# Performance work log

Measured on AMD Instinct MI355X. Metric: run time of the kernel, lower is better.

## Reference

```python
import jax, jax.numpy as jnp
import numpy as np

D_MODEL = 1024
D_STATE = 16
D_CONV = 4
EXPAND = 2
D_INNER = EXPAND * D_MODEL          # 2048
DT_RANK = D_MODEL // 16             # 64
BATCH, SEQ = 4, 2048


def setup_inputs() -> dict:
    key = jax.random.key(0)
    ks = jax.random.split(key, 8)
    s = lambda k, shape, sc=0.02: jax.random.normal(k, shape, jnp.float32) * sc
    x = jax.random.normal(ks[0], (BATCH, SEQ, D_MODEL), jnp.float32)
    tau = jax.random.uniform(ks[1], (BATCH, SEQ), jnp.float32) * 7200.0  # seconds
    # S4D-real init for A
    A_log = jnp.log(jnp.broadcast_to(jnp.arange(1, D_STATE + 1, dtype=jnp.float32), (D_INNER, D_STATE)))
    return dict(
        x=x, tau=tau,
        ln_g=jnp.ones((D_MODEL,), jnp.float32),
        ln_b=jnp.zeros((D_MODEL,), jnp.float32),
        in_proj_w=s(ks[2], (2 * D_INNER, D_MODEL)),
        conv_w=s(ks[3], (D_INNER, 1, D_CONV), 0.1),   # depthwise [O, I/g=1, K]
        conv_b=jnp.zeros((D_INNER,), jnp.float32),
        x_proj_w=s(ks[4], (DT_RANK + 2 * D_STATE, D_INNER)),
        dt_proj_w=s(ks[5], (D_INNER, DT_RANK), 0.1),
        dt_proj_b=jnp.full((D_INNER,), -4.6, jnp.float32),  # softplus ~ 0.01
        A_log=A_log,
        D=jnp.ones((D_INNER,), jnp.float32),
        out_proj_w=s(ks[6], (D_MODEL, D_INNER)),
        log_decay=jnp.full((D_MODEL,), -3.0, jnp.float32),
    )


def _mamba_block(x, tau, ln_g, ln_b, in_proj_w, conv_w, conv_b, x_proj_w,
                 dt_proj_w, dt_proj_b, A_log, D, out_proj_w, log_decay):
    # LayerNorm(d_model)
    mu = jnp.mean(x, axis=-1, keepdims=True)
    var = jnp.var(x, axis=-1, keepdims=True)
    xn = (x - mu) * jax.lax.rsqrt(var + 1e-5) * ln_g + ln_b

    # in_proj -> split into conv branch and gate branch, each [B, L, d_inner]
    xz = jnp.einsum('bld,ed->ble', xn, in_proj_w)
    x_in, z = jnp.split(xz, 2, axis=-1)

    # causal depthwise conv1d over time
    xc = jax.lax.conv_general_dilated(
        x_in.transpose(0, 2, 1), conv_w, (1,), [(D_CONV - 1, 0)],
        dimension_numbers=('NCH', 'OIH', 'NCH'), feature_group_count=D_INNER)
    u = jax.nn.silu(xc.transpose(0, 2, 1) + conv_b)          # [B, L, d_inner]

    # input-dependent SSM params
    x_dbl = jnp.einsum('ble,fe->blf', u, x_proj_w)
    dt, Bm, Cm = jnp.split(x_dbl, [DT_RANK, DT_RANK + D_STATE], axis=-1)
    delta = jax.nn.softplus(jnp.einsum('blr,dr->bld', dt, dt_proj_w) + dt_proj_b)
    A = -jnp.exp(A_log)                                       # [d_inner, d_state]

    # selective scan: h_t = exp(dt*A)*h + dt*u*B_t ; y_t = <h_t, C_t>
    def step(h, inp):
        d_t, B_t, C_t, u_t = inp                              # [B,d],[B,n],[B,n],[B,d]
        h = jnp.exp(d_t[..., None] * A) * h + (d_t * u_t)[..., None] * B_t[:, None, :]
        return h, jnp.einsum('bdn,bn->bd', h, C_t)

    h0 = jnp.zeros((x.shape[0], D_INNER, D_STATE), x.dtype)
    xs = (delta.transpose(1, 0, 2), Bm.transpose(1, 0, 2),
          Cm.transpose(1, 0, 2), u.transpose(1, 0, 2))
    _, ys = jax.lax.scan(step, h0, xs)
    y = ys.transpose(1, 0, 2) + u * D
    y = y * jax.nn.silu(z)
    h_out = jnp.einsum('ble,de->bld', y, out_proj_w)          # mamba output [B,L,d_model]

    # ZOH time-decay gate + residual (dropout = identity in eval)
    tau_h = jnp.maximum(tau / 3600.0, 1e-4)[..., None]
    gate = jnp.exp(-jax.nn.softplus(log_decay) * tau_h)
    return x + h_out * gate


def reference(x, tau, ln_g, ln_b, in_proj_w, conv_w, conv_b, x_proj_w,
              dt_proj_w, dt_proj_b, A_log, D, out_proj_w, log_decay):
    return _mamba_block(x, tau, ln_g, ln_b, in_proj_w, conv_w, conv_b, x_proj_w,
                        dt_proj_w, dt_proj_b, A_log, D, out_proj_w, log_decay)
```

## Files before the change

### kernel.cpp

```cpp
#include <hip/hip_runtime.h>

typedef unsigned short u16;
typedef unsigned int u32;
typedef short s16x8 __attribute__((ext_vector_type(8)));
typedef u16 u16x8 __attribute__((ext_vector_type(8)));
typedef float f32x4 __attribute__((ext_vector_type(4)));

#define TOK 8192
#define DM 1024
#define DI 2048
#define DS 16
#define DR 64
#define NCHUNK 64
#define CH 32
#define XPN 96
#define XP_SPLIT 4
#define CONV_T 16

#define SBAR() do { asm volatile("" ::: "memory"); __builtin_amdgcn_s_barrier(); asm volatile("" ::: "memory"); } while (0)
#define WAITVM(N) do { asm volatile("s_waitcnt vmcnt(" #N ")" ::: "memory"); __builtin_amdgcn_sched_barrier(0); } while (0)
#define WAITLGKM0() do { asm volatile("s_waitcnt lgkmcnt(0)" ::: "memory"); __builtin_amdgcn_sched_barrier(0); } while (0)

__device__ __forceinline__ u16 f2bf(float f) {
    u32 u = __float_as_uint(f);
    u32 r = (u + 0x7fffu + ((u >> 16) & 1u)) >> 16;
    return (u16)r;
}
__device__ __forceinline__ float bf2f(u16 h) {
    return __uint_as_float(((u32)h) << 16);
}
__device__ __forceinline__ float softplus_f(float x) {
    return (x > 15.f) ? x : __logf(1.f + __expf(x));
}
__device__ __forceinline__ void unpack8(const uint4 v, float* o) {
    o[0] = __uint_as_float(v.x << 16); o[1] = __uint_as_float(v.x & 0xffff0000u);
    o[2] = __uint_as_float(v.y << 16); o[3] = __uint_as_float(v.y & 0xffff0000u);
    o[4] = __uint_as_float(v.z << 16); o[5] = __uint_as_float(v.z & 0xffff0000u);
    o[6] = __uint_as_float(v.w << 16); o[7] = __uint_as_float(v.w & 0xffff0000u);
}
__device__ __forceinline__ void async16(u16* lds, const u16* g) {
    __builtin_amdgcn_global_load_lds(
        (const __attribute__((address_space(1))) void*)g,
        (__attribute__((address_space(3))) void*)lds, 16, 0, 0);
}

__global__ __launch_bounds__(256) void cvt_kernel(const float* __restrict__ src,
                                                  u16* __restrict__ dst, int n4) {
    int i = blockIdx.x * 256 + threadIdx.x;
    if (i >= n4) return;
    float4 v = ((const float4*)src)[i];
    ushort4 o;
    o.x = f2bf(v.x); o.y = f2bf(v.y); o.z = f2bf(v.z); o.w = f2bf(v.w);
    ((ushort4*)dst)[i] = o;
}

__global__ __launch_bounds__(256) void prep_kernel(const float* __restrict__ tau,
                                                   const float* __restrict__ log_decay,
                                                   float* __restrict__ th,
                                                   float* __restrict__ sd) {
    int i = blockIdx.x * 256 + threadIdx.x;
    if (i < TOK) th[i] = fmaxf(tau[i] * (1.f / 3600.f), 1e-4f);
    if (i < DM)  sd[i] = softplus_f(log_decay[i]);
}

__global__ __launch_bounds__(256) void ln_kernel(const float* __restrict__ x,
                                                 const float* __restrict__ g,
                                                 const float* __restrict__ bb,
                                                 u16* __restrict__ xn) {
    const int tok = blockIdx.x;
    const float4 v = ((const float4*)(x + (size_t)tok * DM))[threadIdx.x];
    float s = v.x + v.y + v.z + v.w;
    float sq = v.x * v.x + v.y * v.y + v.z * v.z + v.w * v.w;
#pragma unroll
    for (int off = 32; off; off >>= 1) {
        s += __shfl_xor(s, off);
        sq += __shfl_xor(sq, off);
    }
    __shared__ float red[8];
    const int wv = threadIdx.x >> 6;
    if ((threadIdx.x & 63) == 0) { red[wv] = s; red[4 + wv] = sq; }
    __syncthreads();
    s = red[0] + red[1] + red[2] + red[3];
    sq = red[4] + red[5] + red[6] + red[7];
    const float mean = s * (1.f / DM);
    const float var = sq * (1.f / DM) - mean * mean;
    const float rstd = rsqrtf(var + 1e-5f);
    const float4 gv = ((const float4*)g)[threadIdx.x];
    const float4 bv = ((const float4*)bb)[threadIdx.x];
    ushort4 o;
    o.x = f2bf((v.x - mean) * rstd * gv.x + bv.x);
    o.y = f2bf((v.y - mean) * rstd * gv.y + bv.y);
    o.z = f2bf((v.z - mean) * rstd * gv.z + bv.z);
    o.w = f2bf((v.w - mean) * rstd * gv.w + bv.w);
    ((ushort4*)(xn + (size_t)tok * DM))[threadIdx.x] = o;
}

template <int EPI>
__global__ __launch_bounds__(512) void gemm256(
    const u16* __restrict__ A, int lda,
    const u16* __restrict__ W, int ldw, int K,
    u16* __restrict__ Cb, float* __restrict__ Cf, int ldc,
    int MBLK) {
    __shared__ __align__(16) u16 lds[2 * 32768];
    const int tid = threadIdx.x;
    const int wave = tid >> 6, lane = tid & 63;
    const int wm = wave >> 2, wn = wave & 3;
    const int fl = lane & 15, fh = lane >> 4;
    const int cpx = gridDim.x >> 3;
    const int swz = ((int)blockIdx.x & 7) * cpx + ((int)blockIdx.x >> 3);
    const int bm = swz % MBLK, bn = swz / MBLK;
    const int NT = K >> 6;
    const int kb = (int)blockIdx.y * K;

    const int r0 = tid >> 3;
    const int cb = ((tid & 7) ^ (r0 & 7)) << 3;
    const int rA = bm * 256 + r0;
    const int rB = bn * 256 + r0 + (r0 & ~31);

    f32x4 acc[8][4];
#pragma unroll
    for (int m = 0; m < 8; m++)
#pragma unroll
        for (int n = 0; n < 4; n++) acc[m][n] = f32x4{0.f, 0.f, 0.f, 0.f};

    auto stageA = [&](int buf, int h, int k0) {
#pragma unroll
        for (int j = 0; j < 2; j++)
            async16(lds + buf * 32768 + h * 8192 + j * 4096 + tid * 8,
                    A + (size_t)(rA + j * 128 + h * 64) * lda + kb + k0 + cb);
    };
    auto stageB = [&](int buf, int h, int k0) {
#pragma unroll
        for (int j = 0; j < 2; j++)
            async16(lds + buf * 32768 + 16384 + h * 8192 + j * 4096 + tid * 8,
                    W + (size_t)(rB + j * 128 + h * 32) * ldw + kb + k0 + cb);
    };
    auto rdA = [&](int buf, int mf, int kk) -> s16x8 {
        int r = wm * 64 + (mf & 3) * 16 + fl;
        int slot = ((kk << 2) | fh) ^ (fl & 7);
        return *(const s16x8*)(lds + buf * 32768 + (mf >> 2) * 8192 + r * 64 + slot * 8);
    };
    auto rdB = [&](int buf, int nh, int nf, int kk) -> s16x8 {
        int r = wn * 32 + nf * 16 + fl;
        int slot = ((kk << 2) | fh) ^ (fl & 7);
        return *(const s16x8*)(lds + buf * 32768 + 16384 + nh * 8192 + r * 64 + slot * 8);
    };

    stageA(0, 0, 0); stageA(0, 1, 0); stageB(0, 0, 0); stageB(0, 1, 0);
    stageA(1, 0, 64); stageB(1, 0, 64); stageB(1, 1, 64);
    WAITVM(6);
    SBAR();

    for (int t = 0; t < NT; ++t) {
        const int cur = t & 1, nxt = cur ^ 1;
        const int k2 = (t + 2) << 6;
        s16x8 ah[4][2], bh0[2][2], bh1[2][2];
#pragma unroll
        for (int mf = 0; mf < 4; mf++) { ah[mf][0] = rdA(cur, mf, 0); ah[mf][1] = rdA(cur, mf, 1); }
#pragma unroll
        for (int nf = 0; nf < 2; nf++) { bh0[nf][0] = rdB(cur, 0, nf, 0); bh0[nf][1] = rdB(cur, 0, nf, 1); }
        if (t + 1 < NT) stageA(nxt, 1, (t + 1) << 6);
        SBAR();
        WAITLGKM0();
        __builtin_amdgcn_s_setprio(1);
#pragma unroll
        for (int kk = 0; kk < 2; kk++)
#pragma unroll
            for (int mf = 0; mf < 4; mf++)
#pragma unroll
                for (int nf = 0; nf < 2; nf++)
                    acc[mf][nf] = __builtin_amdgcn_mfma_f32_16x16x32_bf16(ah[mf][kk], bh0[nf][kk], acc[mf][nf], 0, 0, 0);
        __builtin_amdgcn_s_setprio(0);
        __builtin_amdgcn_sched_barrier(0);
        SBAR();
#pragma unroll
        for (int nf = 0; nf < 2; nf++) { bh1[nf][0] = rdB(cur, 1, nf, 0); bh1[nf][1] = rdB(cur, 1, nf, 1); }
        if (t + 2 < NT) stageA(cur, 0, k2);
        SBAR();
        WAITLGKM0();
        __builtin_amdgcn_s_setprio(1);
#pragma unroll
        for (int kk = 0; kk < 2; kk++)
#pragma unroll
            for (int mf = 0; mf < 4; mf++)
#pragma unroll
                for (int nf = 0; nf < 2; nf++)
                    acc[mf][2 + nf] = __builtin_amdgcn_mfma_f32_16x16x32_bf16(ah[mf][kk], bh1[nf][kk], acc[mf][2 + nf], 0, 0, 0);
        __builtin_amdgcn_s_setprio(0);
        __builtin_amdgcn_sched_barrier(0);
        SBAR();
#pragma unroll
        for (int mf = 0; mf < 4; mf++) { ah[mf][0] = rdA(cur, 4 + mf, 0); ah[mf][1] = rdA(cur, 4 + mf, 1); }
        if (t + 2 < NT) stageB(cur, 0, k2);
        SBAR();
        WAITLGKM0();
        __builtin_amdgcn_s_setprio(1);
#pragma unroll
        for (int kk = 0; kk < 2; kk++)
#pragma unroll
            for (int mf = 0; mf < 4; mf++)
#pragma unroll
                for (int nf = 0; nf < 2; nf++)
                    acc[4 + mf][2 + nf] = __builtin_amdgcn_mfma_f32_16x16x32_bf16(ah[mf][kk], bh1[nf][kk], acc[4 + mf][2 + nf], 0, 0, 0);
        __builtin_amdgcn_s_setprio(0);
        __builtin_amdgcn_sched_barrier(0);
        SBAR();
        if (t + 2 < NT) { stageB(cur, 1, k2); WAITVM(6); }
        else           { WAITVM(0); }
        SBAR();
        __builtin_amdgcn_s_setprio(1);
#pragma unroll
        for (int kk = 0; kk < 2; kk++)
#pragma unroll
            for (int mf = 0; mf < 4; mf++)
#pragma unroll
                for (int nf = 0; nf < 2; nf++)
                    acc[4 + mf][nf] = __builtin_amdgcn_mfma_f32_16x16x32_bf16(ah[mf][kk], bh0[nf][kk], acc[4 + mf][nf], 0, 0, 0);
        __builtin_amdgcn_s_setprio(0);
        __builtin_amdgcn_sched_barrier(0);
        SBAR();
    }

    float* Cfs = (EPI == 3) ? Cf + (size_t)blockIdx.y * TOK * DM : Cf;
#pragma unroll
    for (int mf = 0; mf < 8; mf++)
#pragma unroll
        for (int j = 0; j < 4; j++) {
            int row = bm * 256 + wm * 128 + mf * 16 + fh * 4 + j;
#pragma unroll
            for (int n = 0; n < 4; n++) {
                int col = bn * 256 + wn * 64 + n * 16 + fl;
                float v = acc[mf][n][j];
                size_t idx = (size_t)row * ldc + col;
                if (EPI == 0) {
                    Cb[idx] = f2bf(v);
                } else {
                    Cfs[idx] = v;
                }
            }
        }
}

__global__ __launch_bounds__(256) void outred(const float* __restrict__ part,
                                              const float* __restrict__ x,
                                              const float* __restrict__ th,
                                              const float* __restrict__ sd,
                                              float* __restrict__ out) {
    const int row = blockIdx.x;
    const float t = th[row];
    const size_t base = (size_t)row * DM + threadIdx.x * 4;
    float4 p0 = *(const float4*)(part + base);
    float4 p1 = *(const float4*)(part + (size_t)TOK * DM + base);
    float4 xr = *(const float4*)(x + base);
    float4 sv = *(const float4*)(sd + threadIdx.x * 4);
    float4 o;
    o.x = xr.x + (p0.x + p1.x) * __expf(-sv.x * t);
    o.y = xr.y + (p0.y + p1.y) * __expf(-sv.y * t);
    o.z = xr.z + (p0.z + p1.z) * __expf(-sv.z * t);
    o.w = xr.w + (p0.w + p1.w) * __expf(-sv.w * t);
    *(float4*)(out + base) = o;
}

template <int EPI>
__global__ __launch_bounds__(256) void gemm_bt(
    const u16* __restrict__ A, int lda,
    const u16* __restrict__ W,
    u16* __restrict__ Cb, float* __restrict__ Cf, int ldc,
    int M, int N, int K,
    const float* __restrict__ bias) {
    __shared__ u16 As[128 * 32];
    __shared__ u16 Bs[128 * 32];
    const int tid = threadIdx.x;
    const int wave = tid >> 6, lane = tid & 63;
    const int bm = blockIdx.x, bn = blockIdx.y;
    const int srow = lane >> 2, scol = (lane & 3) * 8;
    const int wr = wave >> 1, wc = wave & 1;
    const int fl = lane & 15, fh = lane >> 4;

    f32x4 acc[4][4];
#pragma unroll
    for (int m = 0; m < 4; m++)
#pragma unroll
        for (int n = 0; n < 4; n++) acc[m][n] = f32x4{0.f, 0.f, 0.f, 0.f};

    int ra[2], rb[2];
    u16* ldsA[2]; u16* ldsB[2];
#pragma unroll
    for (int i = 0; i < 2; i++) {
        int r = (wave * 2 + i) * 16 + srow;
        ra[i] = min(bm * 128 + r, M - 1);
        rb[i] = min(bn * 128 + r, N - 1);
        ldsA[i] = As + (wave * 2 + i) * 512 + lane * 8;
        ldsB[i] = Bs + (wave * 2 + i) * 512 + lane * 8;
    }

    for (int k0 = 0; k0 < K; k0 += 32) {
        __syncthreads();
#pragma unroll
        for (int i = 0; i < 2; i++) {
            async16(ldsA[i], A + (size_t)ra[i] * lda + k0 + scol);
            async16(ldsB[i], W + (size_t)rb[i] * K + k0 + scol);
        }
        __syncthreads();
        s16x8 av[4], bv[4];
#pragma unroll
        for (int m = 0; m < 4; m++)
            av[m] = *(const s16x8*)(As + (wr * 64 + m * 16 + fl) * 32 + fh * 8);
#pragma unroll
        for (int n = 0; n < 4; n++)
            bv[n] = *(const s16x8*)(Bs + (wc * 64 + n * 16 + fl) * 32 + fh * 8);
#pragma unroll
        for (int m = 0; m < 4; m++)
#pragma unroll
            for (int n = 0; n < 4; n++)
                acc[m][n] = __builtin_amdgcn_mfma_f32_16x16x32_bf16(av[m], bv[n], acc[m][n], 0, 0, 0);
    }

#pragma unroll
    for (int m = 0; m < 4; m++) {
#pragma unroll
        for (int j = 0; j < 4; j++) {
            int row = bm * 128 + wr * 64 + m * 16 + fh * 4 + j;
            if (row >= M) continue;
#pragma unroll
            for (int n = 0; n < 4; n++) {
                int col = bn * 128 + wc * 64 + n * 16 + fl;
                if (col >= N) continue;
                float v = acc[m][n][j];
                size_t idx = (size_t)row * ldc + col;
                if (EPI == 0) {
                    Cb[idx] = f2bf(v);
                } else {
                    Cb[idx] = f2bf(softplus_f(v + bias[col]));
                }
            }
        }
    }
}

__global__ __launch_bounds__(256) void xp_gemm(const u16* __restrict__ A,
                                               const u16* __restrict__ W,
                                               float* __restrict__ part) {
    __shared__ u16 As[128 * 64];
    __shared__ u16 Bs[XPN * 64];
    const int tid = threadIdx.x;
    const int wave = tid >> 6, lane = tid & 63;
    const int bm = blockIdx.x, sp = blockIdx.y;
    const int fl = lane & 15, fh = lane >> 4;
    const int trow = tid >> 3, tcol = (tid & 7) * 8;

    f32x4 acc[2][6];
#pragma unroll
    for (int m = 0; m < 2; m++)
#pragma unroll
        for (int n = 0; n < 6; n++) acc[m][n] = f32x4{0.f, 0.f, 0.f, 0.f};

    const int kbeg = sp * (DI / XP_SPLIT);
    for (int k0 = kbeg; k0 < kbeg + DI / XP_SPLIT; k0 += 64) {
        __syncthreads();
#pragma unroll
        for (int i = 0; i < 4; i++)
            async16(As + i * 2048 + tid * 8,
                    A + (size_t)(bm * 128 + i * 32 + trow) * DI + k0 + tcol);
#pragma unroll
        for (int i = 0; i < 3; i++)
            async16(Bs + i * 2048 + tid * 8,
                    W + (size_t)(i * 32 + trow) * DI + k0 + tcol);
        __syncthreads();
#pragma unroll
        for (int kk = 0; kk < 2; kk++) {
            s16x8 av[2], bv[6];
#pragma unroll
            for (int m = 0; m < 2; m++)
                av[m] = *(const s16x8*)(As + (wave * 32 + m * 16 + fl) * 64 + kk * 32 + fh * 8);
#pragma unroll
            for (int n = 0; n < 6; n++)
                bv[n] = *(const s16x8*)(Bs + (n * 16 + fl) * 64 + kk * 32 + fh * 8);
#pragma unroll
            for (int m = 0; m < 2; m++)
#pragma unroll
                for (int n = 0; n < 6; n++)
                    acc[m][n] = __builtin_amdgcn_mfma_f32_16x16x32_bf16(av[m], bv[n], acc[m][n], 0, 0, 0);
        }
    }
    float* dst = part + (size_t)sp * TOK * XPN;
#pragma unroll
    for (int m = 0; m < 2; m++)
#pragma unroll
        for (int j = 0; j < 4; j++) {
            int row = bm * 128 + wave * 32 + m * 16 + fh * 4 + j;
#pragma unroll
            for (int n = 0; n < 6; n++) {
                int col = n * 16 + fl;
                dst[(size_t)row * XPN + col] = acc[m][n][j];
            }
        }
}

__global__ __launch_bounds__(256) void xp_reduce(const float* __restrict__ part,
                                                 u16* __restrict__ out) {
    int i = blockIdx.x * 256 + threadIdx.x;
    if (i >= TOK * XPN) return;
    float s = 0.f;
#pragma unroll
    for (int sp = 0; sp < XP_SPLIT; sp++) s += part[(size_t)sp * TOK * XPN + i];
    out[i] = f2bf(s);
}

__global__ __launch_bounds__(256) void conv_silu_kernel(const u16* __restrict__ xz,
                                                        const float* __restrict__ cw,
                                                        const float* __restrict__ cb,
                                                        u16* __restrict__ u) {
    const int b = blockIdx.y;
    const int l0 = blockIdx.x * CONV_T;
    const int d0 = threadIdx.x * 8;
    float w0[8], w1[8], w2[8], w3[8], bias[8];
#pragma unroll
    for (int e = 0; e < 8; e++) {
        float4 wv = ((const float4*)cw)[d0 + e];
        w0[e] = wv.x; w1[e] = wv.y; w2[e] = wv.z; w3[e] = wv.w;
        bias[e] = cb[d0 + e];
    }
    float win[4][8];
#pragma unroll
    for (int i = 0; i < 3; i++) {
        int l = l0 - 3 + i;
        int slot = (l0 + 1 + i) & 3;
        if (l < 0) {
#pragma unroll
            for (int e = 0; e < 8; e++) win[slot][e] = 0.f;
        } else {
            u16x8 v = *(const u16x8*)(xz + ((size_t)(b * 2048 + l)) * (2 * DI) + d0);
#pragma unroll
            for (int e = 0; e < 8; e++) win[slot][e] = bf2f(v[e]);
        }
    }
#pragma unroll
    for (int t = 0; t < CONV_T; t++) {
        const int l = l0 + t;
        const size_t tok = (size_t)b * 2048 + l;
        u16x8 v = *(const u16x8*)(xz + tok * (2 * DI) + d0);
        const int s3 = t & 3;
#pragma unroll
        for (int e = 0; e < 8; e++) win[s3][e] = bf2f(v[e]);
        const int s0 = (t + 1) & 3, s1 = (t + 2) & 3, s2 = (t + 3) & 3;
        u16x8 o;
#pragma unroll
        for (int e = 0; e < 8; e++) {
            float a = bias[e];
            a = fmaf(w0[e], win[s0][e], a);
            a = fmaf(w1[e], win[s1][e], a);
            a = fmaf(w2[e], win[s2][e], a);
            a = fmaf(w3[e], win[s3][e], a);
            o[e] = f2bf(a / (1.f + __expf(-a)));
        }
        *(u16x8*)(u + tok * DI + d0) = o;
    }
}

__global__ __launch_bounds__(256) void scan_passA(const u16* __restrict__ delta,
                                                  const u16* __restrict__ u,
                                                  const u16* __restrict__ xdbl,
                                                  const float* __restrict__ A_log,
                                                  float* __restrict__ qh,
                                                  float* __restrict__ Sarr) {
    const int d = blockIdx.x * 256 + threadIdx.x;
    const int b = blockIdx.y, c = blockIdx.z;
    float Av[16];
#pragma unroll
    for (int n = 0; n < 16; n++) Av[n] = -__expf(A_log[d * 16 + n]);
    bool fast = true;
#pragma unroll
    for (int n = 0; n < 16; n++) fast = fast && (fabsf(Av[n] + (float)(n + 1)) < 1e-4f * (n + 1));
    const bool allfast = __all(fast);

    float h[16];
#pragma unroll
    for (int n = 0; n < 16; n++) h[n] = 0.f;
    float S = 0.f;
    const int l0 = c * CH;
    size_t tok = (size_t)b * 2048 + l0;
    float dt = bf2f(delta[tok * DI + d]);
    float uu = bf2f(u[tok * DI + d]);
    const uint4* bp0 = (const uint4*)(xdbl + tok * 96 + 64);
    uint4 b0 = bp0[0], b1 = bp0[1];
    for (int t = 0; t < CH; ++t) {
        const int tn = (t + 1 < CH) ? t + 1 : t;
        const size_t tokn = (size_t)b * 2048 + l0 + tn;
        float dt_n = bf2f(delta[tokn * DI + d]);
        float uu_n = bf2f(u[tokn * DI + d]);
        const uint4* bpn = (const uint4*)(xdbl + tokn * 96 + 64);
        uint4 b0n = bpn[0], b1n = bpn[1];
        float du = dt * uu;
        float Bv[16];
        unpack8(b0, Bv); unpack8(b1, Bv + 8);
        float e[16];
        if (allfast) {
            float r = __expf(-dt);
            e[0] = r;
#pragma unroll
            for (int n = 1; n < 16; n++) e[n] = e[n - 1] * r;
        } else {
#pragma unroll
            for (int n = 0; n < 16; n++) e[n] = __expf(dt * Av[n]);
        }
#pragma unroll
        for (int n = 0; n < 16; n++) h[n] = fmaf(e[n], h[n], du * Bv[n]);
        S += dt;
        dt = dt_n; uu = uu_n; b0 = b0n; b1 = b1n;
    }
    const size_t base = ((size_t)(c * 4 + b) * 16) * DI + d;
#pragma unroll
    for (int n = 0; n < 16; n++) qh[base + (size_t)n * DI] = h[n];
    Sarr[(size_t)(c * 4 + b) * DI + d] = S;
}

__global__ __launch_bounds__(256) void scan_passB(float* __restrict__ qh,
                                                  const float* __restrict__ Sarr,
                                                  const float* __restrict__ A_log) {
    const int idx = blockIdx.x * 256 + threadIdx.x;
    const int d = idx & (DI - 1);
    const int n = (idx >> 11) & 15;
    const int b = idx >> 15;
    const float Avn = -__expf(A_log[d * 16 + n]);
    float h = 0.f;
    for (int c = 0; c < NCHUNK; c++) {
        const size_t base = ((size_t)(c * 4 + b) * 16 + n) * DI + d;
        const float qv = qh[base];
        const float S = Sarr[(size_t)(c * 4 + b) * DI + d];
        qh[base] = h;
        h = fmaf(__expf(Avn * S), h, qv);
    }
}

__global__ __launch_bounds__(256) void scan_passC(const u16* __restrict__ delta,
                                                  const u16* __restrict__ u,
                                                  const u16* __restrict__ xdbl,
                                                  const u16* __restrict__ xz,
                                                  const float* __restrict__ A_log,
                                                  const float* __restrict__ Dvec,
                                                  const float* __restrict__ qh,
                                                  u16* __restrict__ yg) {
    const int d = blockIdx.x * 256 + threadIdx.x;
    const int b = blockIdx.y, c = blockIdx.z;
    float Av[16];
#pragma unroll
    for (int n = 0; n < 16; n++) Av[n] = -__expf(A_log[d * 16 + n]);
    bool fast = true;
#pragma unroll
    for (int n = 0; n < 16; n++) fast = fast && (fabsf(Av[n] + (float)(n + 1)) < 1e-4f * (n + 1));
    const bool allfast = __all(fast);
    const float Dd = Dvec[d];

    float h[16];
    const size_t hbase = ((size_t)(c * 4 + b) * 16) * DI + d;
#pragma unroll
    for (int n = 0; n < 16; n++) h[n] = qh[hbase + (size_t)n * DI];

    const int l0 = c * CH;
    size_t tok = (size_t)b * 2048 + l0;
    float dt = bf2f(delta[tok * DI + d]);
    float uu = bf2f(u[tok * DI + d]);
    float zz = bf2f(xz[tok * (2 * DI) + DI + d]);
    const uint4* bp0 = (const uint4*)(xdbl + tok * 96 + 64);
    uint4 b0 = bp0[0], b1 = bp0[1], c0 = bp0[2], c1 = bp0[3];
    for (int t = 0; t < CH; ++t) {
        const int tn = (t + 1 < CH) ? t + 1 : t;
        const size_t tokn = (size_t)b * 2048 + l0 + tn;
        float dt_n = bf2f(delta[tokn * DI + d]);
        float uu_n = bf2f(u[tokn * DI + d]);
        float zz_n = bf2f(xz[tokn * (2 * DI) + DI + d]);
        const uint4* bpn = (const uint4*)(xdbl + tokn * 96 + 64);
        uint4 b0n = bpn[0], b1n = bpn[1], c0n = bpn[2], c1n = bpn[3];

        float du = dt * uu;
        float Bv[16], Cv[16];
        unpack8(b0, Bv); unpack8(b1, Bv + 8);
        unpack8(c0, Cv); unpack8(c1, Cv + 8);
        float e[16];
        if (allfast) {
            float r = __expf(-dt);
            e[0] = r;
#pragma unroll
            for (int n = 1; n < 16; n++) e[n] = e[n - 1] * r;
        } else {
#pragma unroll
            for (int n = 0; n < 16; n++) e[n] = __expf(dt * Av[n]);
        }
        float y = 0.f;
#pragma unroll
        for (int n = 0; n < 16; n++) {
            h[n] = fmaf(e[n], h[n], du * Bv[n]);
            y = fmaf(h[n], Cv[n], y);
        }
        float sz = zz / (1.f + __expf(-zz));
        const size_t tokc = (size_t)b * 2048 + l0 + t;
        yg[tokc * DI + d] = f2bf((y + uu * Dd) * sz);

        dt = dt_n; uu = uu_n; zz = zz_n;
        b0 = b0n; b1 = b1n; c0 = c0n; c1 = c1n;
    }
}

extern "C" void kernel_launch(void* const* d_in, const int* in_sizes, int n_in,
                              void* d_out, int out_size, void* d_ws, size_t ws_size,
                              hipStream_t stream) {
    const float* x = (const float*)d_in[0];
    const float* tau = (const float*)d_in[1];
    const float* ln_g = (const float*)d_in[2];
    const float* ln_b = (const float*)d_in[3];
    const float* in_proj_w = (const float*)d_in[4];
    const float* conv_w = (const float*)d_in[5];
    const float* conv_b = (const float*)d_in[6];
    const float* x_proj_w = (const float*)d_in[7];
    const float* dt_proj_w = (const float*)d_in[8];
    const float* dt_proj_b = (const float*)d_in[9];
    const float* A_log = (const float*)d_in[10];
    const float* Dvec = (const float*)d_in[11];
    const float* out_proj_w = (const float*)d_in[12];
    const float* log_decay = (const float*)d_in[13];
    float* out = (float*)d_out;

    char* ws = (char*)d_ws;
    size_t off = 0;
    auto alloc = [&](size_t bytes) -> void* {
        void* p = ws + off;
        off += (bytes + 255) & ~(size_t)255;
        return p;
    };
    u16* xn    = (u16*)alloc((size_t)TOK * DM * 2);
    u16* w_in  = (u16*)alloc((size_t)2 * DI * DM * 2);
    u16* w_xp  = (u16*)alloc((size_t)XPN * DI * 2);
    u16* w_dt  = (u16*)alloc((size_t)DI * DR * 2);
    u16* w_out = (u16*)alloc((size_t)DM * DI * 2);
    u16* xz    = (u16*)alloc((size_t)TOK * 2 * DI * 2);
    u16* u     = (u16*)alloc((size_t)TOK * DI * 2);
    u16* xdbl  = (u16*)alloc((size_t)TOK * XPN * 2);
    u16* delta = (u16*)alloc((size_t)TOK * DI * 2);
    float* qh   = (float*)alloc((size_t)NCHUNK * 4 * 16 * DI * 4);
    float* Sarr = (float*)alloc((size_t)NCHUNK * 4 * DI * 4);
    u16* yg    = (u16*)alloc((size_t)TOK * DI * 2);
    float* th = (float*)alloc((size_t)TOK * 4);
    float* sd = (float*)alloc((size_t)DM * 4);
    float* xp_part = (float*)xn;
    float* op_part = (float*)xz;

    cvt_kernel<<<4096, 256, 0, stream>>>(in_proj_w, w_in, (2 * DI * DM) / 4);
    cvt_kernel<<<192, 256, 0, stream>>>(x_proj_w, w_xp, (XPN * DI) / 4);
    cvt_kernel<<<128, 256, 0, stream>>>(dt_proj_w, w_dt, (DI * DR) / 4);
    cvt_kernel<<<2048, 256, 0, stream>>>(out_proj_w, w_out, (DM * DI) / 4);
    prep_kernel<<<32, 256, 0, stream>>>(tau, log_decay, th, sd);

    ln_kernel<<<TOK, 256, 0, stream>>>(x, ln_g, ln_b, xn);

    gemm256<0><<<dim3(512, 1), 512, 0, stream>>>(xn, DM, w_in, DM, DM, xz, nullptr, 2 * DI, 32);
    conv_silu_kernel<<<dim3(2048 / CONV_T, 4), 256, 0, stream>>>(xz, conv_w, conv_b, u);

    xp_gemm<<<dim3(64, XP_SPLIT), 256, 0, stream>>>(u, w_xp, xp_part);
    xp_reduce<<<(TOK * XPN + 255) / 256, 256, 0, stream>>>(xp_part, xdbl);

    gemm_bt<1><<<dim3(64, 16), 256, 0, stream>>>(xdbl, XPN, w_dt, delta, nullptr, DI,
                                                 TOK, DI, DR, dt_proj_b);

    scan_passA<<<dim3(8, 4, NCHUNK), 256, 0, stream>>>(delta, u, xdbl, A_log, qh, Sarr);
    scan_passB<<<512, 256, 0, stream>>>(qh, Sarr, A_log);
    scan_passC<<<dim3(8, 4, NCHUNK), 256, 0, stream>>>(delta, u, xdbl, xz, A_log, Dvec, qh, yg);

    gemm256<3><<<dim3(128, 2), 512, 0, stream>>>(yg, DI, w_out, DI, DI / 2, nullptr, op_part, DM, 32);
    outred<<<TOK, 256, 0, stream>>>(op_part, x, th, sd, out);
}
```

Before: 333.9 us.

## Fuse out-proj epilogue, drop split-K, merge conversion kernels, reorder in-proj tiles

Replaces the split-K out-projection GEMM plus its separate reduction kernel with a new 256x128-tile GEMM that runs the full K and applies the residual add and time-decay gate in its epilogue. This removes the fp32 partial-sum round trip and one launch. The four weight-conversion launches and the prep kernel become a single kernel. The in-proj GEMM's block swizzle now walks N fastest instead of M. The out-proj now runs 256 blocks over the full K, which may reduce parallelism and latency hiding compared with 256 split-K blocks of half the depth.

```diff
diff --git a/kernel.cpp b/kernel.cpp
--- a/kernel.cpp
+++ b/kernel.cpp
@@ -44,23 +44,28 @@
         (__attribute__((address_space(3))) void*)lds, 16, 0, 0);
 }
 
-__global__ __launch_bounds__(256) void cvt_kernel(const float* __restrict__ src,
-                                                  u16* __restrict__ dst, int n4) {
-    int i = blockIdx.x * 256 + threadIdx.x;
-    if (i >= n4) return;
+__global__ __launch_bounds__(256) void cvt_all(
+    const float* __restrict__ in_w, const float* __restrict__ xp_w,
+    const float* __restrict__ dt_w, const float* __restrict__ out_w,
+    const float* __restrict__ tau, const float* __restrict__ log_decay,
+    u16* __restrict__ wi, u16* __restrict__ wxp, u16* __restrict__ wdt,
+    u16* __restrict__ wout, float* __restrict__ th, float* __restrict__ sd) {
+    const int b = blockIdx.x;
+    const float* src; u16* dst; int i;
+    if (b < 4096)      { src = in_w;  dst = wi;   i = b * 256 + threadIdx.x; }
+    else if (b < 4288) { src = xp_w;  dst = wxp;  i = (b - 4096) * 256 + threadIdx.x; }
+    else if (b < 4416) { src = dt_w;  dst = wdt;  i = (b - 4288) * 256 + threadIdx.x; }
+    else if (b < 6464) { src = out_w; dst = wout; i = (b - 4416) * 256 + threadIdx.x; }
+    else {
+        int j = (b - 6464) * 256 + threadIdx.x;
+        if (j < TOK) th[j] = fmaxf(tau[j] * (1.f / 3600.f), 1e-4f);
+        if (j < DM)  sd[j] = softplus_f(log_decay[j]);
+        return;
+    }
     float4 v = ((const float4*)src)[i];
     ushort4 o;
     o.x = f2bf(v.x); o.y = f2bf(v.y); o.z = f2bf(v.z); o.w = f2bf(v.w);
     ((ushort4*)dst)[i] = o;
-}
-
-__global__ __launch_bounds__(256) void prep_kernel(const float* __restrict__ tau,
-                                                   const float* __restrict__ log_decay,
-                                                   float* __restrict__ th,
-                                                   float* __restrict__ sd) {
-    int i = blockIdx.x * 256 + threadIdx.x;
-    if (i < TOK) th[i] = fmaxf(tau[i] * (1.f / 3600.f), 1e-4f);
-    if (i < DM)  sd[i] = softplus_f(log_decay[i]);
 }
 
 __global__ __launch_bounds__(256) void ln_kernel(const float* __restrict__ x,
@@ -95,12 +100,11 @@
     ((ushort4*)(xn + (size_t)tok * DM))[threadIdx.x] = o;
 }
 
-template <int EPI>
 __global__ __launch_bounds__(512) void gemm256(
     const u16* __restrict__ A, int lda,
     const u16* __restrict__ W, int ldw, int K,
-    u16* __restrict__ Cb, float* __restrict__ Cf, int ldc,
-    int MBLK) {
+    u16* __restrict__ Cb, int ldc,
+    int NBLK) {
     __shared__ __align__(16) u16 lds[2 * 32768];
     const int tid = threadIdx.x;
     const int wave = tid >> 6, lane = tid & 63;
@@ -108,9 +112,8 @@
     const int fl = lane & 15, fh = lane >> 4;
     const int cpx = gridDim.x >> 3;
     const int swz = ((int)blockIdx.x & 7) * cpx + ((int)blockIdx.x >> 3);
-    const int bm = swz % MBLK, bn = swz / MBLK;
+    const int bn = swz % NBLK, bm = swz / NBLK;
     const int NT = K >> 6;
-    const int kb = (int)blockIdx.y * K;
 
     const int r0 = tid >> 3;
     const int cb = ((tid & 7) ^ (r0 & 7)) << 3;
@@ -127,13 +130,13 @@
 #pragma unroll
         for (int j = 0; j < 2; j++)
             async16(lds + buf * 32768 + h * 8192 + j * 4096 + tid * 8,
-                    A + (size_t)(rA + j * 128 + h * 64) * lda + kb + k0 + cb);
+                    A + (size_t)(rA + j * 128 + h * 64) * lda + k0 + cb);
     };
     auto stageB = [&](int buf, int h, int k0) {
 #pragma unroll
         for (int j = 0; j < 2; j++)
             async16(lds + buf * 32768 + 16384 + h * 8192 + j * 4096 + tid * 8,
-                    W + (size_t)(rB + j * 128 + h * 32) * ldw + kb + k0 + cb);
+                    W + (size_t)(rB + j * 128 + h * 32) * ldw + k0 + cb);
     };
     auto rdA = [&](int buf, int mf, int kk) -> s16x8 {
         int r = wm * 64 + (mf & 3) * 16 + fl;
@@ -221,7 +224,6 @@
         SBAR();
     }
 
-    float* Cfs = (EPI == 3) ? Cf + (size_t)blockIdx.y * TOK * DM : Cf;
 #pragma unroll
     for (int mf = 0; mf < 8; mf++)
 #pragma unroll
@@ -230,42 +232,146 @@
 #pragma unroll
             for (int n = 0; n < 4; n++) {
                 int col = bn * 256 + wn * 64 + n * 16 + fl;
-                float v = acc[mf][n][j];
+                Cb[(size_t)row * ldc + col] = f2bf(acc[mf][n][j]);
+            }
+        }
+}
+
+__global__ __launch_bounds__(512) void gemm_out(
+    const u16* __restrict__ A, int lda,
+    const u16* __restrict__ W, int ldw, int K,
+    float* __restrict__ Cf, int ldc,
+    int NBLK,
+    const float* __restrict__ xres, const float* __restrict__ th,
+    const float* __restrict__ sd) {
+    __shared__ __align__(16) u16 lds[2 * 24576];
+    const int tid = threadIdx.x;
+    const int wave = tid >> 6, lane = tid & 63;
+    const int wm = wave >> 2, wn = wave & 3;
+    const int fl = lane & 15, fh = lane >> 4;
+    const int cpx = gridDim.x >> 3;
+    const int swz = ((int)blockIdx.x & 7) * cpx + ((int)blockIdx.x >> 3);
+    const int bn = swz % NBLK, bm = swz / NBLK;
+    const int NT = K >> 6;
+
+    const int r0 = tid >> 3;
+    const int cb = ((tid & 7) ^ (r0 & 7)) << 3;
+    const int rA = bm * 256 + r0;
+    const int rB = bn * 128 + r0;
+
+    f32x4 acc[8][2];
+#pragma unroll
+    for (int m = 0; m < 8; m++)
+#pragma unroll
+        for (int n = 0; n < 2; n++) acc[m][n] = f32x4{0.f, 0.f, 0.f, 0.f};
+
+    auto stageA = [&](int buf, int h, int k0) {
+#pragma unroll
+        for (int j = 0; j < 2; j++)
+            async16(lds + buf * 24576 + h * 8192 + j * 4096 + tid * 8,
+                    A + (size_t)(rA + j * 128 + h * 64) * lda + k0 + cb);
+    };
+    auto stageB = [&](int buf, int k0) {
+#pragma unroll
+        for (int j = 0; j < 2; j++)
+            async16(lds + buf * 24576 + 16384 + j * 4096 + tid * 8,
+                    W + (size_t)(rB + j * 64) * ldw + k0 + cb);
+    };
+    auto rdA = [&](int buf, int mf, int kk) -> s16x8 {
+        int r = wm * 64 + (mf & 3) * 16 + fl;
+        int slot = ((kk << 2) | fh) ^ (fl & 7);
+        return *(const s16x8*)(lds + buf * 24576 + (mf >> 2) * 8192 + r * 64 + slot * 8);
+    };
+    auto rdB = [&](int buf, int nf, int kk) -> s16x8 {
+        int r = wn * 32 + nf * 16 + fl;
+        int slot = ((kk << 2) | fh) ^ (fl & 7);
+        return *(const s16x8*)(lds + buf * 24576 + 16384 + r * 64 + slot * 8);
+    };
+
+    stageA(0, 0, 0); stageA(0, 1, 0); stageB(0, 0);
+    stageA(1, 0, 64); stageB(1, 64);
+    WAITVM(4);
+    SBAR();
+
+    for (int t = 0; t < NT; ++t) {
+        const int cur = t & 1, nxt = cur ^ 1;
+        const int k2 = (t + 2) << 6;
+        s16x8 ah[4][2], bh0[2], bh1[2];
+#pragma unroll
+        for (int mf = 0; mf < 4; mf++) { ah[mf][0] = rdA(cur, mf, 0); ah[mf][1] = rdA(cur, mf, 1); }
+        bh0[0] = rdB(cur, 0, 0); bh0[1] = rdB(cur, 0, 1);
+        if (t + 1 < NT) stageA(nxt, 1, (t + 1) << 6);
+        SBAR();
+        WAITLGKM0();
+        __builtin_amdgcn_s_setprio(1);
+#pragma unroll
+        for (int kk = 0; kk < 2; kk++)
+#pragma unroll
+            for (int mf = 0; mf < 4; mf++)
+                acc[mf][0] = __builtin_amdgcn_mfma_f32_16x16x32_bf16(ah[mf][kk], bh0[kk], acc[mf][0], 0, 0, 0);
+        __builtin_amdgcn_s_setprio(0);
+        __builtin_amdgcn_sched_barrier(0);
+        SBAR();
+        bh1[0] = rdB(cur, 1, 0); bh1[1] = rdB(cur, 1, 1);
+        if (t + 2 < NT) stageA(cur, 0, k2);
+        SBAR();
+        WAITLGKM0();
+        __builtin_amdgcn_s_setprio(1);
+#pragma unroll
+        for (int kk = 0; kk < 2; kk++)
+#pragma unroll
+            for (int mf = 0; mf < 4; mf++)
+                acc[mf][1] = __builtin_amdgcn_mfma_f32_16x16x32_bf16(ah[mf][kk], bh1[kk], acc[mf][1], 0, 0, 0);
+        __builtin_amdgcn_s_setprio(0);
+        __builtin_amdgcn_sched_barrier(0);
+        SBAR();
+#pragma unroll
+        for (int mf = 0; mf < 4; mf++) { ah[mf][0] = rdA(cur, 4 + mf, 0); ah[mf][1] = rdA(cur, 4 + mf, 1); }
+        if (t + 2 < NT) stageB(cur, k2);
+        SBAR();
+        WAITLGKM0();
+        __builtin_amdgcn_s_setprio(1);
+#pragma unroll
+        for (int kk = 0; kk < 2; kk++)
+#pragma unroll
+            for (int mf = 0; mf < 4; mf++)
+                acc[4 + mf][1] = __builtin_amdgcn_mfma_f32_16x16x32_bf16(ah[mf][kk], bh1[kk], acc[4 + mf][1], 0, 0, 0);
+        __builtin_amdgcn_s_setprio(0);
+        __builtin_amdgcn_sched_barrier(0);
+        SBAR();
+        if (t + 2 < NT) { WAITVM(4); }
+        else           { WAITVM(0); }
+        SBAR();
+        __builtin_amdgcn_s_setprio(1);
+#pragma unroll
+        for (int kk = 0; kk < 2; kk++)
+#pragma unroll
+            for (int mf = 0; mf < 4; mf++)
+                acc[4 + mf][0] = __builtin_amdgcn_mfma_f32_16x16x32_bf16(ah[mf][kk], bh0[kk], acc[4 + mf][0], 0, 0, 0);
+        __builtin_amdgcn_s_setprio(0);
+        __builtin_amdgcn_sched_barrier(0);
+        SBAR();
+    }
+
+#pragma unroll
+    for (int mf = 0; mf < 8; mf++)
+#pragma unroll
+        for (int j = 0; j < 4; j++) {
+            int row = bm * 256 + wm * 128 + mf * 16 + fh * 4 + j;
+            float t = th[row];
+#pragma unroll
+            for (int n = 0; n < 2; n++) {
+                int col = bn * 128 + wn * 32 + n * 16 + fl;
                 size_t idx = (size_t)row * ldc + col;
-                if (EPI == 0) {
-                    Cb[idx] = f2bf(v);
-                } else {
-                    Cfs[idx] = v;
-                }
+                Cf[idx] = xres[idx] + acc[mf][n][j] * __expf(-sd[col] * t);
             }
         }
 }
 
-__global__ __launch_bounds__(256) void outred(const float* __restrict__ part,
-                                              const float* __restrict__ x,
-                                              const float* __restrict__ th,
-                                              const float* __restrict__ sd,
-                                              float* __restrict__ out) {
-    const int row = blockIdx.x;
-    const float t = th[row];
-    const size_t base = (size_t)row * DM + threadIdx.x * 4;
-    float4 p0 = *(const float4*)(part + base);
-    float4 p1 = *(const float4*)(part + (size_t)TOK * DM + base);
-    float4 xr = *(const float4*)(x + base);
-    float4 sv = *(const float4*)(sd + threadIdx.x * 4);
-    float4 o;
-    o.x = xr.x + (p0.x + p1.x) * __expf(-sv.x * t);
-    o.y = xr.y + (p0.y + p1.y) * __expf(-sv.y * t);
-    o.z = xr.z + (p0.z + p1.z) * __expf(-sv.z * t);
-    o.w = xr.w + (p0.w + p1.w) * __expf(-sv.w * t);
-    *(float4*)(out + base) = o;
-}
-
-template <int EPI>
 __global__ __launch_bounds__(256) void gemm_bt(
     const u16* __restrict__ A, int lda,
     const u16* __restrict__ W,
-    u16* __restrict__ Cb, float* __restrict__ Cf, int ldc,
+    u16* __restrict__ Cb, int ldc,
     int M, int N, int K,
     const float* __restrict__ bias) {
     __shared__ u16 As[128 * 32];
@@ -326,13 +432,7 @@
             for (int n = 0; n < 4; n++) {
                 int col = bn * 128 + wc * 64 + n * 16 + fl;
                 if (col >= N) continue;
-                float v = acc[m][n][j];
-                size_t idx = (size_t)row * ldc + col;
-                if (EPI == 0) {
-                    Cb[idx] = f2bf(v);
-                } else {
-                    Cb[idx] = f2bf(softplus_f(v + bias[col]));
-                }
+                Cb[(size_t)row * ldc + col] = f2bf(softplus_f(acc[m][n][j] + bias[col]));
             }
         }
     }
@@ -643,29 +743,24 @@
     float* th = (float*)alloc((size_t)TOK * 4);
     float* sd = (float*)alloc((size_t)DM * 4);
     float* xp_part = (float*)xn;
-    float* op_part = (float*)xz;
-
-    cvt_kernel<<<4096, 256, 0, stream>>>(in_proj_w, w_in, (2 * DI * DM) / 4);
-    cvt_kernel<<<192, 256, 0, stream>>>(x_proj_w, w_xp, (XPN * DI) / 4);
-    cvt_kernel<<<128, 256, 0, stream>>>(dt_proj_w, w_dt, (DI * DR) / 4);
-    cvt_kernel<<<2048, 256, 0, stream>>>(out_proj_w, w_out, (DM * DI) / 4);
-    prep_kernel<<<32, 256, 0, stream>>>(tau, log_decay, th, sd);
+
+    cvt_all<<<6496, 256, 0, stream>>>(in_proj_w, x_proj_w, dt_proj_w, out_proj_w,
+                                      tau, log_decay, w_in, w_xp, w_dt, w_out, th, sd);
 
     ln_kernel<<<TOK, 256, 0, stream>>>(x, ln_g, ln_b, xn);
 
-    gemm256<0><<<dim3(512, 1), 512, 0, stream>>>(xn, DM, w_in, DM, DM, xz, nullptr, 2 * DI, 32);
+    gemm256<<<512, 512, 0, stream>>>(xn, DM, w_in, DM, DM, xz, 2 * DI, 16);
     conv_silu_kernel<<<dim3(2048 / CONV_T, 4), 256, 0, stream>>>(xz, conv_w, conv_b, u);
 
     xp_gemm<<<dim3(64, XP_SPLIT), 256, 0, stream>>>(u, w_xp, xp_part);
     xp_reduce<<<(TOK * XPN + 255) / 256, 256, 0, stream>>>(xp_part, xdbl);
 
-    gemm_bt<1><<<dim3(64, 16), 256, 0, stream>>>(xdbl, XPN, w_dt, delta, nullptr, DI,
-                                                 TOK, DI, DR, dt_proj_b);
+    gemm_bt<<<dim3(64, 16), 256, 0, stream>>>(xdbl, XPN, w_dt, delta, DI,
+                                              TOK, DI, DR, dt_proj_b);
 
     scan_passA<<<dim3(8, 4, NCHUNK), 256, 0, stream>>>(delta, u, xdbl, A_log, qh, Sarr);
     scan_passB<<<512, 256, 0, stream>>>(qh, Sarr, A_log);
     scan_passC<<<dim3(8, 4, NCHUNK), 256, 0, stream>>>(delta, u, xdbl, xz, A_log, Dvec, qh, yg);
 
-    gemm256<3><<<dim3(128, 2), 512, 0, stream>>>(yg, DI, w_out, DI, DI / 2, nullptr, op_part, DM, 32);
-    outred<<<TOK, 256, 0, stream>>>(op_part, x, th, sd, out);
-}
+    gemm_out<<<256, 512, 0, stream>>>(yg, DI, w_out, DI, DI, out, DM, 8, x, th, sd);
+}
```

Measured after the change: 313.2 us. 1.07x faster.
